# Kernel tuning notes

Measured on AMD Instinct MI355X. Metric: run time of the kernel, lower is better.

## Reference

```python
import jax, jax.numpy as jnp
import numpy as np

N_NODES = 50000
N_EDGES = 800000
D_IN = 128
HIDDEN = 64
N_CLASSES = 2


def gcn_conv(x, edge_index, W, b, num_nodes):
    """PyG GCNConv: linear (no bias) -> add self-loops -> sym-normalized aggregate -> + bias."""
    h = x @ W  # [N, H]
    loop = jnp.arange(num_nodes, dtype=edge_index.dtype)
    src = jnp.concatenate([edge_index[0], loop])  # [E+N]
    dst = jnp.concatenate([edge_index[1], loop])
    deg = jax.ops.segment_sum(jnp.ones_like(dst, dtype=h.dtype), dst, num_segments=num_nodes)
    dinv = jnp.where(deg > 0, jax.lax.rsqrt(deg), 0.0)
    norm = dinv[src] * dinv[dst]  # [E+N]
    msg = h[src] * norm[:, None]  # [E+N, H]  (gather + scale)
    out = jax.ops.segment_sum(msg, dst, num_segments=num_nodes)  # scatter-add
    return out + b


def setup_inputs() -> dict:
    key = jax.random.key(0)
    ks = jax.random.split(key, 6)
    x = jax.random.normal(ks[0], (N_NODES, D_IN), dtype=jnp.float32)
    edge_index = jax.random.randint(ks[1], (2, N_EDGES), 0, N_NODES, dtype=jnp.int64)
    # Glorot-ish init for weights, zero bias (PyG default)
    W1 = jax.random.normal(ks[2], (D_IN, HIDDEN), dtype=jnp.float32) * (1.0 / np.sqrt(D_IN))
    b1 = jnp.zeros((HIDDEN,), dtype=jnp.float32)
    W2 = jax.random.normal(ks[3], (HIDDEN, N_CLASSES), dtype=jnp.float32) * (1.0 / np.sqrt(HIDDEN))
    b2 = jnp.zeros((N_CLASSES,), dtype=jnp.float32)
    return {"x": x, "edge_index": edge_index, "W1": W1, "b1": b1, "W2": W2, "b2": b2}


def reference(x, edge_index, W1, b1, W2, b2):
    h = jax.nn.relu(gcn_conv(x, edge_index, W1, b1, N_NODES))
    # F.dropout(training=self.training) is identity in eval mode
    out = gcn_conv(h, edge_index, W2, b2, N_NODES)
    return out
```

## Files before the change

### kernel.cpp

```cpp
#include <hip/hip_runtime.h>

#define N_NODES 50000
#define N_EDGES 800000
#define D_IN 128
#define HIDDEN 64
#define N_CLASSES 2
#define NBUK 782
#define NBUK_P 784
#define NBLK 196
#define NBLK_P 200
#define NE4 200000
#define XPAD 136

typedef _Float16 half4v __attribute__((ext_vector_type(4)));
typedef _Float16 h8 __attribute__((ext_vector_type(8)));
typedef float f4 __attribute__((ext_vector_type(4)));


__global__ __launch_bounds__(256) void k_hist_gemm(
    const int4* __restrict__ dst4, int* __restrict__ bhist,
    const float* __restrict__ x, const float* __restrict__ W1,
    _Float16* __restrict__ hs)
{
    __shared__ __attribute__((aligned(16))) _Float16 smem[2 * 64 * XPAD];
    const int t = threadIdx.x;

    if (blockIdx.x < NBLK) {
        int* hist = (int*)smem;
        for (int i = t; i < NBUK_P; i += 256) hist[i] = 0;
        __syncthreads();
        int base4 = blockIdx.x * 1024;
#pragma unroll
        for (int k = 0; k < 4; k++) {
            int idx = base4 + k * 256 + t;
            if (idx < NE4) {
                int4 d = dst4[idx];
                atomicAdd(&hist[d.x >> 6], 1);
                atomicAdd(&hist[d.y >> 6], 1);
                atomicAdd(&hist[d.z >> 6], 1);
                atomicAdd(&hist[d.w >> 6], 1);
            }
        }
        __syncthreads();
        for (int i = t; i < NBUK_P; i += 256) bhist[blockIdx.x * NBUK_P + i] = hist[i];
        return;
    }

    _Float16* xs = smem;
    _Float16* Wt = smem + 64 * XPAD;
    const int gb = blockIdx.x - NBLK;
    const int row0 = gb * 64;

    for (int i4 = t; i4 < 64 * D_IN / 4; i4 += 256) {
        int r = i4 >> 5;
        int k4 = (i4 & 31) << 2;
        int grow = row0 + r;
        half4v hv;
        if (grow < N_NODES) {
            float4 v = *(const float4*)&x[grow * D_IN + k4];
            hv.x = (_Float16)v.x; hv.y = (_Float16)v.y;
            hv.z = (_Float16)v.z; hv.w = (_Float16)v.w;
        } else {
            hv.x = hv.y = hv.z = hv.w = (_Float16)0.f;
        }
        *(half4v*)&xs[r * XPAD + k4] = hv;
    }
    for (int i4 = t; i4 < D_IN * HIDDEN / 4; i4 += 256) {
        float4 v = *(const float4*)&W1[i4 * 4];
        int k = i4 >> 4;
        int n = (i4 & 15) << 2;
        Wt[(n + 0) * XPAD + k] = (_Float16)v.x;
        Wt[(n + 1) * XPAD + k] = (_Float16)v.y;
        Wt[(n + 2) * XPAD + k] = (_Float16)v.z;
        Wt[(n + 3) * XPAD + k] = (_Float16)v.w;
    }
    __syncthreads();

    const int w = t >> 6;
    const int L = t & 63;
    const int mrow = w * 16 + (L & 15);
    const int qk = (L >> 4) * 8;
    f4 acc0 = {0.f, 0.f, 0.f, 0.f}, acc1 = acc0, acc2 = acc0, acc3 = acc0;
#pragma unroll
    for (int ks = 0; ks < D_IN; ks += 32) {
        h8 a  = *(const h8*)&xs[mrow * XPAD + ks + qk];
        h8 b0 = *(const h8*)&Wt[(0 * 16 + (L & 15)) * XPAD + ks + qk];
        h8 b1 = *(const h8*)&Wt[(1 * 16 + (L & 15)) * XPAD + ks + qk];
        h8 b2 = *(const h8*)&Wt[(2 * 16 + (L & 15)) * XPAD + ks + qk];
        h8 b3 = *(const h8*)&Wt[(3 * 16 + (L & 15)) * XPAD + ks + qk];
        acc0 = __builtin_amdgcn_mfma_f32_16x16x32_f16(a, b0, acc0, 0, 0, 0);
        acc1 = __builtin_amdgcn_mfma_f32_16x16x32_f16(a, b1, acc1, 0, 0, 0);
        acc2 = __builtin_amdgcn_mfma_f32_16x16x32_f16(a, b2, acc2, 0, 0, 0);
        acc3 = __builtin_amdgcn_mfma_f32_16x16x32_f16(a, b3, acc3, 0, 0, 0);
    }

    const int n0 = L & 15;
#pragma unroll
    for (int j = 0; j < 4; j++) {
        int m = w * 16 + (L >> 4) * 4 + j;
        size_t base = (size_t)(row0 + m) * HIDDEN;
        hs[base + 0 * 16 + n0] = (_Float16)acc0[j];
        hs[base + 1 * 16 + n0] = (_Float16)acc1[j];
        hs[base + 2 * 16 + n0] = (_Float16)acc2[j];
        hs[base + 3 * 16 + n0] = (_Float16)acc3[j];
    }
}


__global__ __launch_bounds__(256) void k_colscan(const int* __restrict__ bhist,
                                                 int* __restrict__ excT,
                                                 int* __restrict__ colsum) {
    __shared__ int part[256];
    int b = blockIdx.x;
    int t = threadIdx.x;
    int v = (t < NBLK) ? bhist[t * NBUK_P + b] : 0;
    part[t] = v;
    __syncthreads();
    for (int off = 1; off < 256; off <<= 1) {
        int p = (t >= off) ? part[t - off] : 0;
        __syncthreads();
        part[t] += p;
        __syncthreads();
    }
    if (t < NBLK) excT[b * NBLK_P + t] = part[t] - v;
    if (t == 255) colsum[b] = part[255];
}


__global__ __launch_bounds__(256) void k_binA2s(const int4* __restrict__ src4,
                                                const int4* __restrict__ dst4,
                                                const int* __restrict__ excT,
                                                const int* __restrict__ colsum,
                                                int* __restrict__ bucket_off,
                                                int* __restrict__ row_ptr,
                                                int* __restrict__ ebin) {
    __shared__ int part[256];
    __shared__ int cur[NBUK];
    const int b = blockIdx.x;
    const int t = threadIdx.x;

    int v[4];
    int s = 0;
#pragma unroll
    for (int i = 0; i < 4; i++) {
        int idx = t * 4 + i;
        v[i] = (idx < NBUK) ? colsum[idx] : 0;
        s += v[i];
    }
    part[t] = s;
    __syncthreads();
    for (int off = 1; off < 256; off <<= 1) {
        int p = (t >= off) ? part[t - off] : 0;
        __syncthreads();
        part[t] += p;
        __syncthreads();
    }
    int run = (t == 0) ? 0 : part[t - 1];
#pragma unroll
    for (int i = 0; i < 4; i++) {
        int idx = t * 4 + i;
        if (idx < NBUK) {
            cur[idx] = run + excT[idx * NBLK_P + b];
            if (b == 0) bucket_off[idx] = run;
            run += v[i];
        } else if (idx == NBUK && b == 0) {
            bucket_off[idx] = run;
        }
    }
    if (b == 0 && t == 0) row_ptr[N_NODES] = N_EDGES;
    __syncthreads();

    int base4 = b * 1024;
#pragma unroll
    for (int k = 0; k < 4; k++) {
        int idx = base4 + k * 256 + t;
        if (idx < NE4) {
            int4 sv = src4[idx];
            int4 d = dst4[idx];
            int p0 = atomicAdd(&cur[d.x >> 6], 1);
            int p1 = atomicAdd(&cur[d.y >> 6], 1);
            int p2 = atomicAdd(&cur[d.z >> 6], 1);
            int p3 = atomicAdd(&cur[d.w >> 6], 1);
            ebin[p0] = (sv.x << 7) | (d.x & 63);
            ebin[p1] = (sv.y << 7) | (d.y & 63);
            ebin[p2] = (sv.z << 7) | (d.z & 63);
            ebin[p3] = (sv.w << 7) | (d.w & 63);
        }
    }
}


__global__ __launch_bounds__(256) void k_csr_scale(
    const int* __restrict__ ebin, const int* __restrict__ bucket_off,
    int* __restrict__ row_ptr, float* __restrict__ dinv_g,
    int* __restrict__ rec, _Float16* __restrict__ hs)
{
    __shared__ int cnt[64];
    __shared__ int cur[64];
    __shared__ float sdinv[64];
    const int b = blockIdx.x;
    const int t = threadIdx.x;
    const int row0 = b * 64;

    if (t < 64) cnt[t] = 0;
    __syncthreads();
    int beg = bucket_off[b], end = bucket_off[b + 1];
    for (int i = beg + t; i < end; i += 256) atomicAdd(&cnt[ebin[i] & 63], 1);
    __syncthreads();
    if (t < 64) {
        int deg = cnt[t];
        int sum = deg;
#pragma unroll
        for (int off = 1; off < 64; off <<= 1) {
            int v = __shfl_up(sum, off, 64);
            if (t >= off) sum += v;
        }
        int rp = beg + sum - deg;
        cur[t] = rp;
        float di = rsqrtf((float)(deg + 1));
        sdinv[t] = di;
        int node = row0 + t;
        if (node < N_NODES) {
            row_ptr[node] = rp;
            dinv_g[node] = di;
        }
    }
    __syncthreads();
    for (int i = beg + t; i < end; i += 256) {
        int pk = ebin[i];
        int pos = atomicAdd(&cur[pk & 63], 1);
        rec[pos] = pk >> 7;
    }
    for (int i = t; i < 64 * HIDDEN / 8; i += 256) {
        int r = i >> 3;
        int c = (i & 7) << 3;
        size_t base = (size_t)(row0 + r) * HIDDEN + c;
        h8 hv = *(const h8*)&hs[base];
        float di = sdinv[r];
#pragma unroll
        for (int k = 0; k < 8; k++) hv[k] = (_Float16)((float)hv[k] * di);
        *(h8*)&hs[base] = hv;
    }
}


__global__ __launch_bounds__(256) void k_agg1_l2(
    const _Float16* __restrict__ hs, const int* __restrict__ row_ptr,
    const int* __restrict__ rec, const float* __restrict__ dinv,
    const float* __restrict__ b1, const float* __restrict__ W2,
    float* __restrict__ zs)
{
    const int node = blockIdx.x * 16 + (threadIdx.x >> 4);
    const int g = threadIdx.x & 15;
    const int gbase = threadIdx.x & 48;
    const half4v* H = (const half4v*)hs;

    float di = dinv[node];
    float4 acc = make_float4(0.f, 0.f, 0.f, 0.f);

    int beg = row_ptr[node];
    int end = row_ptr[node + 1];

    for (int base = beg; base < end; base += 16) {
        int n = end - base;
        if (n > 16) n = 16;
        int r = N_NODES;
        if (g < n) r = rec[base + g];
        int n8 = (n + 7) & ~7;
        for (int e = 0; e < n8; e += 8) {
            int i0 = gbase + e;
            int s0 = __shfl(r, i0 + 0, 64);
            int s1 = __shfl(r, i0 + 1, 64);
            int s2 = __shfl(r, i0 + 2, 64);
            int s3 = __shfl(r, i0 + 3, 64);
            int s4 = __shfl(r, i0 + 4, 64);
            int s5 = __shfl(r, i0 + 5, 64);
            int s6 = __shfl(r, i0 + 6, 64);
            int s7 = __shfl(r, i0 + 7, 64);
            half4v a0 = H[s0 * 16 + g];
            half4v a1 = H[s1 * 16 + g];
            half4v a2 = H[s2 * 16 + g];
            half4v a3 = H[s3 * 16 + g];
            half4v a4 = H[s4 * 16 + g];
            half4v a5 = H[s5 * 16 + g];
            half4v a6 = H[s6 * 16 + g];
            half4v a7 = H[s7 * 16 + g];
            acc.x += ((float)a0.x + (float)a1.x) + ((float)a2.x + (float)a3.x)
                   + ((float)a4.x + (float)a5.x) + ((float)a6.x + (float)a7.x);
            acc.y += ((float)a0.y + (float)a1.y) + ((float)a2.y + (float)a3.y)
                   + ((float)a4.y + (float)a5.y) + ((float)a6.y + (float)a7.y);
            acc.z += ((float)a0.z + (float)a1.z) + ((float)a2.z + (float)a3.z)
                   + ((float)a4.z + (float)a5.z) + ((float)a6.z + (float)a7.z);
            acc.w += ((float)a0.w + (float)a1.w) + ((float)a2.w + (float)a3.w)
                   + ((float)a4.w + (float)a5.w) + ((float)a6.w + (float)a7.w);
        }
    }

    half4v sv = H[node * 16 + g];
    acc.x += (float)sv.x;
    acc.y += (float)sv.y;
    acc.z += (float)sv.z;
    acc.w += (float)sv.w;

    float4 bb = ((const float4*)b1)[g];
    float4 y;
    y.x = fmaxf(fmaf(acc.x, di, bb.x), 0.f);
    y.y = fmaxf(fmaf(acc.y, di, bb.y), 0.f);
    y.z = fmaxf(fmaf(acc.z, di, bb.z), 0.f);
    y.w = fmaxf(fmaf(acc.w, di, bb.w), 0.f);
    float4 wA = ((const float4*)W2)[2 * g];
    float4 wB = ((const float4*)W2)[2 * g + 1];
    float p0 = y.x * wA.x + y.y * wA.z + y.z * wB.x + y.w * wB.z;
    float p1 = y.x * wA.y + y.y * wA.w + y.z * wB.y + y.w * wB.w;

    p0 += __shfl_down(p0, 8, 64);
    p1 += __shfl_down(p1, 8, 64);
    p0 += __shfl_down(p0, 4, 64);
    p1 += __shfl_down(p1, 4, 64);
    p0 += __shfl_down(p0, 2, 64);
    p1 += __shfl_down(p1, 2, 64);
    p0 += __shfl_down(p0, 1, 64);
    p1 += __shfl_down(p1, 1, 64);
    if (g == 0) {
        zs[node * 2 + 0] = p0 * di;
        zs[node * 2 + 1] = p1 * di;
    }
}


__global__ __launch_bounds__(256) void k_agg2(
    const float* __restrict__ zs, const int* __restrict__ row_ptr,
    const int* __restrict__ rec, const float* __restrict__ dinv,
    const float* __restrict__ b2, float* __restrict__ out)
{
    const int node = blockIdx.x * 32 + (threadIdx.x >> 3);
    const int j = threadIdx.x & 7;
    if (node >= N_NODES) return;
    int beg = row_ptr[node];
    int end = row_ptr[node + 1];
    float a0 = 0.f, a1 = 0.f;
    for (int idx = beg + j; idx < end; idx += 8) {
        int s = rec[idx];
        float2 v = *(const float2*)&zs[s * 2];
        a0 += v.x;
        a1 += v.y;
    }
    a0 += __shfl_down(a0, 4, 64);
    a1 += __shfl_down(a1, 4, 64);
    a0 += __shfl_down(a0, 2, 64);
    a1 += __shfl_down(a1, 2, 64);
    a0 += __shfl_down(a0, 1, 64);
    a1 += __shfl_down(a1, 1, 64);
    if (j == 0) {
        float di = dinv[node];
        float2 zv = *(const float2*)&zs[node * 2];
        float2 o;
        o.x = fmaf(di, a0 + zv.x, b2[0]);
        o.y = fmaf(di, a1 + zv.y, b2[1]);
        *(float2*)&out[node * 2] = o;
    }
}


extern "C" void kernel_launch(void* const* d_in, const int* in_sizes, int n_in,
                              void* d_out, int out_size, void* d_ws, size_t ws_size,
                              hipStream_t stream) {
    const float* x  = (const float*)d_in[0];
    const int* ei   = (const int*)d_in[1];
    const float* W1 = (const float*)d_in[2];
    const float* b1 = (const float*)d_in[3];
    const float* W2 = (const float*)d_in[4];
    const float* b2 = (const float*)d_in[5];
    float* out = (float*)d_out;

    const int4* src4 = (const int4*)ei;
    const int4* dst4 = (const int4*)(ei + N_EDGES);

    int*      bucket_off = (int*)d_ws;
    int*      colsum     = (int*)d_ws + 1024;
    float*    dinv       = (float*)d_ws + 2048;
    int*      row_ptr    = (int*)d_ws + 52224;
    int*      bhist      = (int*)d_ws + 102432;
    int*      excT       = (int*)d_ws + 256128;
    int*      ebin       = (int*)d_ws + 412576;
    int*      rec        = (int*)d_ws + 1212576;
    _Float16* hs         = (_Float16*)((int*)d_ws + 2012576);
    float*    zs         = (float*)d_ws + 3614112;

    k_hist_gemm<<<NBLK + NBUK, 256, 0, stream>>>(dst4, bhist, x, W1, hs);
    k_colscan<<<NBUK, 256, 0, stream>>>(bhist, excT, colsum);
    k_binA2s<<<NBLK, 256, 0, stream>>>(src4, dst4, excT, colsum, bucket_off, row_ptr, ebin);
    k_csr_scale<<<NBUK, 256, 0, stream>>>(ebin, bucket_off, row_ptr, dinv, rec, hs);
    k_agg1_l2<<<N_NODES / 16, 256, 0, stream>>>(hs, row_ptr, rec, dinv, b1, W2, zs);
    k_agg2<<<(N_NODES + 31) / 32, 256, 0, stream>>>(zs, row_ptr, rec, dinv, b2, out);
}
```

Baseline: 128.9 us.

## Compute degrees globally, fuse scaling into colscan and CSR build into layer-1 aggregation

Per-node in-degrees are now counted with global atomics inside the histogram pass. This lets the hs scaling by dinv move into the column-scan kernel. The CSR bucket sort is fused with the layer-1 aggregation in a 1024-thread block per 64-node bucket, which keeps the source list in shared memory when it fits (CAP) and falls back to global rec otherwise. The aim is to drop one kernel launch and one global round trip of rec. The cost is an extra memset, 800k global atomics, and bigger blocks with a large shared-memory footprint that may lower occupancy.

```diff
diff --git a/kernel.cpp b/kernel.cpp
--- a/kernel.cpp
+++ b/kernel.cpp
@@ -11,6 +11,7 @@
 #define NBLK_P 200
 #define NE4 200000
 #define XPAD 136
+#define CAP 2048
 
 typedef _Float16 half4v __attribute__((ext_vector_type(4)));
 typedef _Float16 h8 __attribute__((ext_vector_type(8)));
@@ -19,6 +20,7 @@
 
 __global__ __launch_bounds__(256) void k_hist_gemm(
     const int4* __restrict__ dst4, int* __restrict__ bhist,
+    int* __restrict__ deg,
     const float* __restrict__ x, const float* __restrict__ W1,
     _Float16* __restrict__ hs)
 {
@@ -39,6 +41,10 @@
                 atomicAdd(&hist[d.y >> 6], 1);
                 atomicAdd(&hist[d.z >> 6], 1);
                 atomicAdd(&hist[d.w >> 6], 1);
+                atomicAdd(&deg[d.x], 1);
+                atomicAdd(&deg[d.y], 1);
+                atomicAdd(&deg[d.z], 1);
+                atomicAdd(&deg[d.w], 1);
             }
         }
         __syncthreads();
@@ -107,12 +113,20 @@
 }
 
 
-__global__ __launch_bounds__(256) void k_colscan(const int* __restrict__ bhist,
-                                                 int* __restrict__ excT,
-                                                 int* __restrict__ colsum) {
+__global__ __launch_bounds__(256) void k_colscan_scale(
+    const int* __restrict__ bhist, const int* __restrict__ deg,
+    int* __restrict__ excT, int* __restrict__ colsum,
+    float* __restrict__ dinv_g, _Float16* __restrict__ hs)
+{
     __shared__ int part[256];
-    int b = blockIdx.x;
-    int t = threadIdx.x;
+    __shared__ float sdv[64];
+    const int b = blockIdx.x;
+    const int t = threadIdx.x;
+    const int row0 = b * 64;
+
+    int dg = 0;
+    if (t < 64) dg = deg[row0 + t];
+
     int v = (t < NBLK) ? bhist[t * NBUK_P + b] : 0;
     part[t] = v;
     __syncthreads();
@@ -124,6 +138,24 @@
     }
     if (t < NBLK) excT[b * NBLK_P + t] = part[t] - v;
     if (t == 255) colsum[b] = part[255];
+
+    if (t < 64) {
+        float di = rsqrtf((float)dg + 1.f);
+        sdv[t] = di;
+        int node = row0 + t;
+        if (node < N_NODES) dinv_g[node] = di;
+    }
+    __syncthreads();
+    for (int i = t; i < 64 * HIDDEN / 8; i += 256) {
+        int r = i >> 3;
+        int c = (i & 7) << 3;
+        size_t base = (size_t)(row0 + r) * HIDDEN + c;
+        h8 hv = *(const h8*)&hs[base];
+        float di = sdv[r];
+#pragma unroll
+        for (int k = 0; k < 8; k++) hv[k] = (_Float16)((float)hv[k] * di);
+        *(h8*)&hs[base] = hv;
+    }
 }
 
 
@@ -190,82 +222,62 @@
 }
 
 
-__global__ __launch_bounds__(256) void k_csr_scale(
+__global__ __launch_bounds__(1024) void k_csr_agg1(
     const int* __restrict__ ebin, const int* __restrict__ bucket_off,
-    int* __restrict__ row_ptr, float* __restrict__ dinv_g,
-    int* __restrict__ rec, _Float16* __restrict__ hs)
+    const int* __restrict__ deg, const _Float16* __restrict__ hs,
+    const float* __restrict__ b1, const float* __restrict__ W2,
+    int* __restrict__ row_ptr, int* __restrict__ rec, float* __restrict__ zs)
 {
-    __shared__ int cnt[64];
+    __shared__ int lrec[CAP];
     __shared__ int cur[64];
-    __shared__ float sdinv[64];
+    __shared__ int lstart[65];
+    __shared__ float sdv[64];
     const int b = blockIdx.x;
     const int t = threadIdx.x;
     const int row0 = b * 64;
-
-    if (t < 64) cnt[t] = 0;
-    __syncthreads();
-    int beg = bucket_off[b], end = bucket_off[b + 1];
-    for (int i = beg + t; i < end; i += 256) atomicAdd(&cnt[ebin[i] & 63], 1);
-    __syncthreads();
+    const int beg = bucket_off[b], end = bucket_off[b + 1];
+    const bool ovf = (end - beg) > CAP;
+
     if (t < 64) {
-        int deg = cnt[t];
-        int sum = deg;
+        int dg = deg[row0 + t];
+        int sum = dg;
 #pragma unroll
         for (int off = 1; off < 64; off <<= 1) {
-            int v = __shfl_up(sum, off, 64);
-            if (t >= off) sum += v;
-        }
-        int rp = beg + sum - deg;
-        cur[t] = rp;
-        float di = rsqrtf((float)(deg + 1));
-        sdinv[t] = di;
+            int vv = __shfl_up(sum, off, 64);
+            if (t >= off) sum += vv;
+        }
+        int ex = sum - dg;
+        cur[t] = ex;
+        lstart[t] = ex;
+        if (t == 63) lstart[64] = sum;
+        sdv[t] = rsqrtf((float)dg + 1.f);
         int node = row0 + t;
-        if (node < N_NODES) {
-            row_ptr[node] = rp;
-            dinv_g[node] = di;
-        }
-    }
-    __syncthreads();
-    for (int i = beg + t; i < end; i += 256) {
+        if (node < N_NODES) row_ptr[node] = beg + ex;
+    }
+    __syncthreads();
+    for (int i = beg + t; i < end; i += 1024) {
         int pk = ebin[i];
-        int pos = atomicAdd(&cur[pk & 63], 1);
-        rec[pos] = pk >> 7;
-    }
-    for (int i = t; i < 64 * HIDDEN / 8; i += 256) {
-        int r = i >> 3;
-        int c = (i & 7) << 3;
-        size_t base = (size_t)(row0 + r) * HIDDEN + c;
-        h8 hv = *(const h8*)&hs[base];
-        float di = sdinv[r];
-#pragma unroll
-        for (int k = 0; k < 8; k++) hv[k] = (_Float16)((float)hv[k] * di);
-        *(h8*)&hs[base] = hv;
-    }
-}
-
-
-__global__ __launch_bounds__(256) void k_agg1_l2(
-    const _Float16* __restrict__ hs, const int* __restrict__ row_ptr,
-    const int* __restrict__ rec, const float* __restrict__ dinv,
-    const float* __restrict__ b1, const float* __restrict__ W2,
-    float* __restrict__ zs)
-{
-    const int node = blockIdx.x * 16 + (threadIdx.x >> 4);
-    const int g = threadIdx.x & 15;
-    const int gbase = threadIdx.x & 48;
+        int p = atomicAdd(&cur[pk & 63], 1);
+        int s = pk >> 7;
+        rec[beg + p] = s;
+        if (p < CAP) lrec[p] = s;
+    }
+    __syncthreads();
+
+    const int g = t & 15;
+    const int gbase = t & 48;
+    const int nl = t >> 4;
+    const int node = row0 + nl;
     const half4v* H = (const half4v*)hs;
-
-    float di = dinv[node];
+    const int ls = lstart[nl], le = lstart[nl + 1];
+    const float di = sdv[nl];
     float4 acc = make_float4(0.f, 0.f, 0.f, 0.f);
 
-    int beg = row_ptr[node];
-    int end = row_ptr[node + 1];
-
-    for (int base = beg; base < end; base += 16) {
-        int n = end - base;
+    for (int base = ls; base < le; base += 16) {
+        int n = le - base;
         if (n > 16) n = 16;
         int r = N_NODES;
-        if (g < n) r = rec[base + g];
+        if (g < n) r = ovf ? rec[beg + base + g] : lrec[base + g];
         int n8 = (n + 7) & ~7;
         for (int e = 0; e < n8; e += 8) {
             int i0 = gbase + e;
@@ -321,7 +333,7 @@
     p1 += __shfl_down(p1, 2, 64);
     p0 += __shfl_down(p0, 1, 64);
     p1 += __shfl_down(p1, 1, 64);
-    if (g == 0) {
+    if (g == 0 && node < N_NODES) {
         zs[node * 2 + 0] = p0 * di;
         zs[node * 2 + 1] = p1 * di;
     }
@@ -386,11 +398,12 @@
     int*      rec        = (int*)d_ws + 1212576;
     _Float16* hs         = (_Float16*)((int*)d_ws + 2012576);
     float*    zs         = (float*)d_ws + 3614112;
-
-    k_hist_gemm<<<NBLK + NBUK, 256, 0, stream>>>(dst4, bhist, x, W1, hs);
-    k_colscan<<<NBUK, 256, 0, stream>>>(bhist, excT, colsum);
+    int*      deg        = (int*)d_ws + 3714112;
+
+    hipMemsetAsync(deg, 0, 50048 * sizeof(int), stream);
+    k_hist_gemm<<<NBLK + NBUK, 256, 0, stream>>>(dst4, bhist, deg, x, W1, hs);
+    k_colscan_scale<<<NBUK, 256, 0, stream>>>(bhist, deg, excT, colsum, dinv, hs);
     k_binA2s<<<NBLK, 256, 0, stream>>>(src4, dst4, excT, colsum, bucket_off, row_ptr, ebin);
-    k_csr_scale<<<NBUK, 256, 0, stream>>>(ebin, bucket_off, row_ptr, dinv, rec, hs);
-    k_agg1_l2<<<N_NODES / 16, 256, 0, stream>>>(hs, row_ptr, rec, dinv, b1, W2, zs);
+    k_csr_agg1<<<NBUK, 1024, 0, stream>>>(ebin, bucket_off, deg, hs, b1, W2, row_ptr, rec, zs);
     k_agg2<<<(N_NODES + 31) / 32, 256, 0, stream>>>(zs, row_ptr, rec, dinv, b2, out);
 }
```

Measured after the change: 162.6 us. 26.2% more time.
